# Kernel tuning notes

Hardware: AMD Instinct MI355X
Metric: run time of the kernel (lower is better)

## Reference

```python
import jax, jax.numpy as jnp
import numpy as np

B, S, D, E, K = 64, 1024, 1024, 8, 2
Z_COEF = 1e-3      # router_z_loss_coef
AUX_COEF = 1e-3    # router_aux_loss_coef


def setup_inputs() -> dict:
    key = jax.random.key(0)
    k1, k2, k3 = jax.random.split(key, 3)
    x = jax.random.normal(k1, (B, S, D), dtype=jnp.float32)
    # xavier-uniform-ish init for query weight, randn for expert keys (as in torch init)
    lim_q = float(np.sqrt(6.0 / (D + D)))
    Wq = jax.random.uniform(k2, (D, D), dtype=jnp.float32, minval=-lim_q, maxval=lim_q)
    bq = jnp.zeros((D,), dtype=jnp.float32)
    lim_k = float(np.sqrt(6.0 / (E + D)))
    key_emb = jax.random.uniform(k3, (E, D), dtype=jnp.float32, minval=-lim_k, maxval=lim_k)
    return {"x": x, "Wq": Wq, "bq": bq, "key_emb": key_emb}


def reference(x, Wq, bq, key_emb):
    b, s, d = x.shape
    e = key_emb.shape[0]
    scale = d ** (-0.5)

    # q = Linear(x); attn over expert keys
    q = jnp.einsum('bsd,od->bso', x, Wq) + bq              # [B,S,D]
    attn_scores = jnp.einsum('bsd,ed->bse', q, key_emb) * scale  # [B,S,E]
    attn_weights = jax.nn.softmax(attn_scores, axis=-1)    # [B,S,E]

    # per-batch expert scores, top-k selection, scatter mask
    scores = attn_weights.mean(axis=1)                     # [B,E]
    top_k_scores, top_k_indices = jax.lax.top_k(scores, K)  # [B,K]
    mask2d = jnp.zeros_like(scores).at[jnp.arange(b)[:, None], top_k_indices].set(1.0)  # [B,E]
    mask = jnp.broadcast_to(mask2d[:, None, :], (b, s, e))  # [B,S,E]

    # routing loss: KL(load-balance) + entropy-style aux
    total_tokens = b * s
    expert_usage_prob = mask2d.sum(axis=0) * (s / total_tokens)   # == mask.sum((0,1))/total
    ideal_prob = jnp.full((e,), 1.0 / e, dtype=scores.dtype)
    # F.kl_div(log_input, target, reduction='batchmean'): sum(t*(log t - log_in))/batch(=E)
    kl = jnp.sum(ideal_prob * (jnp.log(ideal_prob) - jnp.log(expert_usage_prob))) / e
    aux = jnp.mean(attn_weights * jnp.log(attn_weights + 1e-9))
    router_loss = Z_COEF * kl + AUX_COEF * aux

    return mask, top_k_indices, router_loss
```

## Files before the change

### kernel.cpp

```cpp
#include <hip/hip_runtime.h>
#include <math.h>

#define W2OFF  0
#define B2OFF  8192
#define SCOFF  8200
#define AUXOFF 8712
#define ZCNT   513

__global__ __launch_bounds__(256) void k0_prep(const float* __restrict__ bq,
                                               const float* __restrict__ key,
                                               float* __restrict__ ws) {
    __shared__ float part[256 * 8];
    int tid = threadIdx.x;
    #pragma unroll
    for (int k = 0; k < 3; ++k) {
        int i = tid + 256 * k;
        if (i < ZCNT) ws[SCOFF + i] = 0.0f;
    }
    float p[8];
    #pragma unroll
    for (int e = 0; e < 8; ++e) p[e] = 0.0f;
    #pragma unroll
    for (int k = 0; k < 4; ++k) {
        int d = tid + 256 * k;
        float bv = bq[d];
        #pragma unroll
        for (int e = 0; e < 8; ++e) p[e] += bv * key[e * 1024 + d];
    }
    #pragma unroll
    for (int e = 0; e < 8; ++e) part[tid * 8 + e] = p[e];
    __syncthreads();
    if (tid < 8) {
        float s = 0.0f;
        for (int k = 0; k < 256; ++k) s += part[k * 8 + tid];
        ws[B2OFF + tid] = s;
    }
}

__global__ __launch_bounds__(256) void k1_w2(const float* __restrict__ Wq,
                                             const float* __restrict__ key,
                                             float* __restrict__ ws) {
    __shared__ __attribute__((aligned(16))) float keyl[8 * 1024];
    __shared__ float part[256 * 8];
    int tid = threadIdx.x;
    int blk = blockIdx.x;

    float4* kl4 = (float4*)keyl;
    const float4* kg4 = (const float4*)key;
    #pragma unroll
    for (int k = 0; k < 8; ++k) kl4[tid + 256 * k] = kg4[tid + 256 * k];
    __syncthreads();

    int dl = tid & 15;
    int og = tid >> 4;
    int d  = blk * 16 + dl;
    float acc[8];
    #pragma unroll
    for (int e = 0; e < 8; ++e) acc[e] = 0.0f;
    for (int oo = 0; oo < 64; ++oo) {
        int o = og * 64 + oo;
        float wv = Wq[o * 1024 + d];
        #pragma unroll
        for (int e = 0; e < 8; ++e) acc[e] += keyl[e * 1024 + o] * wv;
    }
    #pragma unroll
    for (int e = 0; e < 8; ++e) part[tid * 8 + e] = acc[e];
    __syncthreads();
    if (tid < 128) {
        int dl2 = tid >> 3, e = tid & 7;
        float s = 0.0f;
        #pragma unroll
        for (int g = 0; g < 16; ++g) s += part[(g * 16 + dl2) * 8 + e];
        ws[W2OFF + e * 1024 + blk * 16 + dl2] = s;
    }
}

__global__ __launch_bounds__(256) void k2_main(const float* __restrict__ x,
                                               float* __restrict__ ws) {
    __shared__ __attribute__((aligned(16))) float w2l[8 * 1024];
    __shared__ __attribute__((aligned(16))) float part[4 * 64 * 8];
    __shared__ __attribute__((aligned(16))) float sraw[64 * 8];

    int tid  = threadIdx.x;
    int blk  = blockIdx.x;
    int lane = tid & 63;
    int w    = tid >> 6;
    int batch = blk >> 4;
    int tb    = blk * 64;

    float4* wl4 = (float4*)w2l;
    const float4* wg4 = (const float4*)(ws + W2OFF);
    #pragma unroll
    for (int k = 0; k < 8; ++k) wl4[tid + 256 * k] = wg4[tid + 256 * k];
    __syncthreads();

    const float4* x4 = (const float4*)x;
    float* pw = part + w * 512;

    for (int p = 0; p < 4; ++p) {
        int lt0 = w * 16 + p * 4;
        int t0  = tb + lt0;
        float acc[4][8];
        #pragma unroll
        for (int j = 0; j < 4; ++j)
            #pragma unroll
            for (int e = 0; e < 8; ++e) acc[j][e] = 0.0f;

        #pragma unroll
        for (int i = 0; i < 4; ++i) {
            float4 xr[4];
            #pragma unroll
            for (int j = 0; j < 4; ++j)
                xr[j] = x4[(size_t)(t0 + j) * 256 + i * 64 + lane];
            #pragma unroll
            for (int e = 0; e < 8; ++e) {
                float4 w4 = wl4[e * 256 + i * 64 + lane];
                #pragma unroll
                for (int j = 0; j < 4; ++j)
                    acc[j][e] += w4.x * xr[j].x + w4.y * xr[j].y +
                                 w4.z * xr[j].z + w4.w * xr[j].w;
            }
        }

        #pragma unroll
        for (int j = 0; j < 4; ++j) {
            float4* pw4 = (float4*)(pw + lane * 8);
            pw4[0] = make_float4(acc[j][0], acc[j][1], acc[j][2], acc[j][3]);
            pw4[1] = make_float4(acc[j][4], acc[j][5], acc[j][6], acc[j][7]);
            int e = lane >> 3, r = lane & 7;
            float s = 0.0f;
            #pragma unroll
            for (int m = 0; m < 8; ++m) s += pw[(r + m * 8) * 8 + e];
            s += __shfl_xor(s, 1);
            s += __shfl_xor(s, 2);
            s += __shfl_xor(s, 4);
            if (r == 0) sraw[(lt0 + j) * 8 + e] = s;
        }
    }
    __syncthreads();

    if (tid < 64) {
        float4 a = ((float4*)sraw)[tid * 2];
        float4 b = ((float4*)sraw)[tid * 2 + 1];
        float s[8] = {a.x, a.y, a.z, a.w, b.x, b.y, b.z, b.w};
        const float scale = 0.03125f;
        #pragma unroll
        for (int e = 0; e < 8; ++e) s[e] = (s[e] + ws[B2OFF + e]) * scale;
        float mx = s[0];
        #pragma unroll
        for (int e = 1; e < 8; ++e) mx = fmaxf(mx, s[e]);
        float wgt[8], sum = 0.0f;
        #pragma unroll
        for (int e = 0; e < 8; ++e) { wgt[e] = expf(s[e] - mx); sum += wgt[e]; }
        float inv = 1.0f / sum;
        float aux = 0.0f;
        #pragma unroll
        for (int e = 0; e < 8; ++e) {
            wgt[e] *= inv;
            aux += wgt[e] * logf(wgt[e] + 1e-9f);
        }
        float* pw0 = part;
        float4* q4 = (float4*)(pw0 + tid * 8);
        q4[0] = make_float4(wgt[0], wgt[1], wgt[2], wgt[3]);
        q4[1] = make_float4(wgt[4], wgt[5], wgt[6], wgt[7]);
        int e = tid >> 3, r = tid & 7;
        float s2 = 0.0f;
        #pragma unroll
        for (int m = 0; m < 8; ++m) s2 += pw0[(r + m * 8) * 8 + e];
        s2 += __shfl_xor(s2, 1);
        s2 += __shfl_xor(s2, 2);
        s2 += __shfl_xor(s2, 4);
        if (r == 0) atomicAdd(&ws[SCOFF + batch * 8 + e], s2);
        aux += __shfl_xor(aux, 1);
        aux += __shfl_xor(aux, 2);
        aux += __shfl_xor(aux, 4);
        aux += __shfl_xor(aux, 8);
        aux += __shfl_xor(aux, 16);
        aux += __shfl_xor(aux, 32);
        if (tid == 0) atomicAdd(&ws[AUXOFF], aux);
    }
}

__device__ __forceinline__ void top2_of8(const float* v, int& i1, int& i2) {
    i1 = 0; float b1 = v[0];
    #pragma unroll
    for (int e = 1; e < 8; ++e) if (v[e] > b1) { b1 = v[e]; i1 = e; }
    i2 = -1; float b2 = -3.4e38f;
    #pragma unroll
    for (int e = 0; e < 8; ++e) if (e != i1 && v[e] > b2) { b2 = v[e]; i2 = e; }
}

__global__ __launch_bounds__(256) void k3_out(const float* __restrict__ ws,
                                              float* __restrict__ out) {
    int tid = threadIdx.x;
    int blk = blockIdx.x;
    int batch = blk >> 2;

    float v[8];
    #pragma unroll
    for (int e = 0; e < 8; ++e) v[e] = ws[SCOFF + batch * 8 + e];
    int i1, i2;
    top2_of8(v, i1, i2);

    float m[8];
    #pragma unroll
    for (int e = 0; e < 8; ++e) m[e] = (e == i1 || e == i2) ? 1.0f : 0.0f;
    int token = blk * 256 + tid;
    float4* o4 = (float4*)out;
    o4[token * 2]     = make_float4(m[0], m[1], m[2], m[3]);
    o4[token * 2 + 1] = make_float4(m[4], m[5], m[6], m[7]);

    if (blk == 0) {
        __shared__ int cnt[8];
        if (tid < 8) cnt[tid] = 0;
        __syncthreads();
        if (tid < 64) {
            float vv[8];
            #pragma unroll
            for (int e = 0; e < 8; ++e) vv[e] = ws[SCOFF + tid * 8 + e];
            int j1, j2;
            top2_of8(vv, j1, j2);
            out[524288 + tid * 2]     = (float)j1;
            out[524288 + tid * 2 + 1] = (float)j2;
            atomicAdd(&cnt[j1], 1);
            atomicAdd(&cnt[j2], 1);
        }
        __syncthreads();
        if (tid == 0) {
            float kl = 0.0f;
            #pragma unroll
            for (int e = 0; e < 8; ++e) {
                float usage = (float)cnt[e] / 64.0f;
                kl += 0.125f * (logf(0.125f) - logf(usage));
            }
            kl *= 0.125f;
            float aux = ws[AUXOFF] / 524288.0f;
            out[524416] = 1e-3f * kl + 1e-3f * aux;
        }
    }
}

extern "C" void kernel_launch(void* const* d_in, const int* in_sizes, int n_in,
                              void* d_out, int out_size, void* d_ws, size_t ws_size,
                              hipStream_t stream) {
    const float* x   = (const float*)d_in[0];
    const float* Wq  = (const float*)d_in[1];
    const float* bq  = (const float*)d_in[2];
    const float* key = (const float*)d_in[3];
    float* out = (float*)d_out;
    float* ws  = (float*)d_ws;

    k0_prep<<<1,    256, 0, stream>>>(bq, key, ws);
    k1_w2  <<<64,   256, 0, stream>>>(Wq, key, ws);
    k2_main<<<1024, 256, 0, stream>>>(x, ws);
    k3_out <<<256,  256, 0, stream>>>(ws, out);
}
```

Baseline: 387.7 us.

## Fuse prep kernels and fold top-k/mask output into main kernel via last-block counters

Merges the bias-projection prep into the W2 precompute kernel and folds the softmax, top-2 selection, mask write and loss finalisation into the main x-streaming kernel. The last block per batch, found with an atomic ticket counter, writes that batch's mask, and the last batch finalises the loss. Softmax is now computed per token across lanes with shuffles rather than serially by one wave, and a launch-bounds occupancy hint is added. This removes two kernel launches and a separate pass over the mask, at the cost of atomics, fences and a tail of work in the final blocks.

```diff
diff --git a/kernel.cpp b/kernel.cpp
--- a/kernel.cpp
+++ b/kernel.cpp
@@ -5,46 +5,28 @@
 #define B2OFF  8192
 #define SCOFF  8200
 #define AUXOFF 8712
-#define ZCNT   513
-
-__global__ __launch_bounds__(256) void k0_prep(const float* __restrict__ bq,
-                                               const float* __restrict__ key,
-                                               float* __restrict__ ws) {
-    __shared__ float part[256 * 8];
-    int tid = threadIdx.x;
-    #pragma unroll
-    for (int k = 0; k < 3; ++k) {
-        int i = tid + 256 * k;
-        if (i < ZCNT) ws[SCOFF + i] = 0.0f;
-    }
-    float p[8];
-    #pragma unroll
-    for (int e = 0; e < 8; ++e) p[e] = 0.0f;
-    #pragma unroll
-    for (int k = 0; k < 4; ++k) {
-        int d = tid + 256 * k;
-        float bv = bq[d];
-        #pragma unroll
-        for (int e = 0; e < 8; ++e) p[e] += bv * key[e * 1024 + d];
-    }
-    #pragma unroll
-    for (int e = 0; e < 8; ++e) part[tid * 8 + e] = p[e];
-    __syncthreads();
-    if (tid < 8) {
-        float s = 0.0f;
-        for (int k = 0; k < 256; ++k) s += part[k * 8 + tid];
-        ws[B2OFF + tid] = s;
-    }
-}
-
-__global__ __launch_bounds__(256) void k1_w2(const float* __restrict__ Wq,
-                                             const float* __restrict__ key,
-                                             float* __restrict__ ws) {
+#define TKOFF  8713
+#define GTOFF  8777
+#define CNTOFF 8778
+#define ZTOT   586
+
+__global__ __launch_bounds__(256) void k01_prep(const float* __restrict__ Wq,
+                                                const float* __restrict__ key,
+                                                const float* __restrict__ bq,
+                                                float* __restrict__ ws) {
     __shared__ __attribute__((aligned(16))) float keyl[8 * 1024];
     __shared__ float part[256 * 8];
     int tid = threadIdx.x;
     int blk = blockIdx.x;
 
+    if (blk == 0) {
+        #pragma unroll
+        for (int k = 0; k < 3; ++k) {
+            int i = tid + 256 * k;
+            if (i < ZTOT) ws[SCOFF + i] = 0.0f;
+        }
+    }
+
     float4* kl4 = (float4*)keyl;
     const float4* kg4 = (const float4*)key;
     #pragma unroll
@@ -73,13 +55,44 @@
         for (int g = 0; g < 16; ++g) s += part[(g * 16 + dl2) * 8 + e];
         ws[W2OFF + e * 1024 + blk * 16 + dl2] = s;
     }
-}
-
-__global__ __launch_bounds__(256) void k2_main(const float* __restrict__ x,
-                                               float* __restrict__ ws) {
+
+    if (blk == 0) {
+        __syncthreads();
+        float p[8];
+        #pragma unroll
+        for (int e = 0; e < 8; ++e) p[e] = 0.0f;
+        #pragma unroll
+        for (int k = 0; k < 4; ++k) {
+            int d2 = tid + 256 * k;
+            float bv = bq[d2];
+            #pragma unroll
+            for (int e = 0; e < 8; ++e) p[e] += bv * keyl[e * 1024 + d2];
+        }
+        #pragma unroll
+        for (int e = 0; e < 8; ++e) part[tid * 8 + e] = p[e];
+        __syncthreads();
+        if (tid < 8) {
+            float s = 0.0f;
+            for (int k = 0; k < 256; ++k) s += part[k * 8 + tid];
+            ws[B2OFF + tid] = s;
+        }
+    }
+}
+
+__device__ __forceinline__ void top2_of8(const float* v, int& i1, int& i2) {
+    i1 = 0; float b1 = v[0];
+    #pragma unroll
+    for (int e = 1; e < 8; ++e) if (v[e] > b1) { b1 = v[e]; i1 = e; }
+    i2 = -1; float b2 = -3.4e38f;
+    #pragma unroll
+    for (int e = 0; e < 8; ++e) if (e != i1 && v[e] > b2) { b2 = v[e]; i2 = e; }
+}
+
+__global__ __launch_bounds__(256, 4) void k2_all(const float* __restrict__ x,
+                                                 float* __restrict__ ws,
+                                                 float* __restrict__ out) {
     __shared__ __attribute__((aligned(16))) float w2l[8 * 1024];
     __shared__ __attribute__((aligned(16))) float part[4 * 64 * 8];
-    __shared__ __attribute__((aligned(16))) float sraw[64 * 8];
 
     int tid  = threadIdx.x;
     int blk  = blockIdx.x;
@@ -87,15 +100,19 @@
     int w    = tid >> 6;
     int batch = blk >> 4;
     int tb    = blk * 64;
+    int e = lane >> 3, r = lane & 7;
 
     float4* wl4 = (float4*)w2l;
     const float4* wg4 = (const float4*)(ws + W2OFF);
     #pragma unroll
     for (int k = 0; k < 8; ++k) wl4[tid + 256 * k] = wg4[tid + 256 * k];
+    float b2v = ws[B2OFF + e];
     __syncthreads();
 
     const float4* x4 = (const float4*)x;
     float* pw = part + w * 512;
+    const float scale = 0.03125f;
+    float sc_acc = 0.0f, aux_acc = 0.0f;
 
     for (int p = 0; p < 4; ++p) {
         int lt0 = w * 16 + p * 4;
@@ -104,7 +121,7 @@
         #pragma unroll
         for (int j = 0; j < 4; ++j)
             #pragma unroll
-            for (int e = 0; e < 8; ++e) acc[j][e] = 0.0f;
+            for (int ee = 0; ee < 8; ++ee) acc[j][ee] = 0.0f;
 
         #pragma unroll
         for (int i = 0; i < 4; ++i) {
@@ -113,12 +130,12 @@
             for (int j = 0; j < 4; ++j)
                 xr[j] = x4[(size_t)(t0 + j) * 256 + i * 64 + lane];
             #pragma unroll
-            for (int e = 0; e < 8; ++e) {
-                float4 w4 = wl4[e * 256 + i * 64 + lane];
+            for (int ee = 0; ee < 8; ++ee) {
+                float4 w4 = wl4[ee * 256 + i * 64 + lane];
                 #pragma unroll
                 for (int j = 0; j < 4; ++j)
-                    acc[j][e] += w4.x * xr[j].x + w4.y * xr[j].y +
-                                 w4.z * xr[j].z + w4.w * xr[j].w;
+                    acc[j][ee] += w4.x * xr[j].x + w4.y * xr[j].y +
+                                  w4.z * xr[j].z + w4.w * xr[j].w;
             }
         }
 
@@ -127,114 +144,88 @@
             float4* pw4 = (float4*)(pw + lane * 8);
             pw4[0] = make_float4(acc[j][0], acc[j][1], acc[j][2], acc[j][3]);
             pw4[1] = make_float4(acc[j][4], acc[j][5], acc[j][6], acc[j][7]);
-            int e = lane >> 3, r = lane & 7;
             float s = 0.0f;
             #pragma unroll
             for (int m = 0; m < 8; ++m) s += pw[(r + m * 8) * 8 + e];
             s += __shfl_xor(s, 1);
             s += __shfl_xor(s, 2);
             s += __shfl_xor(s, 4);
-            if (r == 0) sraw[(lt0 + j) * 8 + e] = s;
-        }
-    }
-    __syncthreads();
-
-    if (tid < 64) {
-        float4 a = ((float4*)sraw)[tid * 2];
-        float4 b = ((float4*)sraw)[tid * 2 + 1];
-        float s[8] = {a.x, a.y, a.z, a.w, b.x, b.y, b.z, b.w};
-        const float scale = 0.03125f;
-        #pragma unroll
-        for (int e = 0; e < 8; ++e) s[e] = (s[e] + ws[B2OFF + e]) * scale;
-        float mx = s[0];
-        #pragma unroll
-        for (int e = 1; e < 8; ++e) mx = fmaxf(mx, s[e]);
-        float wgt[8], sum = 0.0f;
-        #pragma unroll
-        for (int e = 0; e < 8; ++e) { wgt[e] = expf(s[e] - mx); sum += wgt[e]; }
-        float inv = 1.0f / sum;
-        float aux = 0.0f;
-        #pragma unroll
-        for (int e = 0; e < 8; ++e) {
-            wgt[e] *= inv;
-            aux += wgt[e] * logf(wgt[e] + 1e-9f);
-        }
-        float* pw0 = part;
-        float4* q4 = (float4*)(pw0 + tid * 8);
-        q4[0] = make_float4(wgt[0], wgt[1], wgt[2], wgt[3]);
-        q4[1] = make_float4(wgt[4], wgt[5], wgt[6], wgt[7]);
-        int e = tid >> 3, r = tid & 7;
-        float s2 = 0.0f;
-        #pragma unroll
-        for (int m = 0; m < 8; ++m) s2 += pw0[(r + m * 8) * 8 + e];
-        s2 += __shfl_xor(s2, 1);
-        s2 += __shfl_xor(s2, 2);
-        s2 += __shfl_xor(s2, 4);
-        if (r == 0) atomicAdd(&ws[SCOFF + batch * 8 + e], s2);
-        aux += __shfl_xor(aux, 1);
-        aux += __shfl_xor(aux, 2);
-        aux += __shfl_xor(aux, 4);
-        aux += __shfl_xor(aux, 8);
-        aux += __shfl_xor(aux, 16);
-        aux += __shfl_xor(aux, 32);
-        if (tid == 0) atomicAdd(&ws[AUXOFF], aux);
-    }
-}
-
-__device__ __forceinline__ void top2_of8(const float* v, int& i1, int& i2) {
-    i1 = 0; float b1 = v[0];
-    #pragma unroll
-    for (int e = 1; e < 8; ++e) if (v[e] > b1) { b1 = v[e]; i1 = e; }
-    i2 = -1; float b2 = -3.4e38f;
-    #pragma unroll
-    for (int e = 0; e < 8; ++e) if (e != i1 && v[e] > b2) { b2 = v[e]; i2 = e; }
-}
-
-__global__ __launch_bounds__(256) void k3_out(const float* __restrict__ ws,
-                                              float* __restrict__ out) {
-    int tid = threadIdx.x;
-    int blk = blockIdx.x;
-    int batch = blk >> 2;
-
+            float sv = (s + b2v) * scale;
+            float mx = sv;
+            mx = fmaxf(mx, __shfl_xor(mx, 8));
+            mx = fmaxf(mx, __shfl_xor(mx, 16));
+            mx = fmaxf(mx, __shfl_xor(mx, 32));
+            float ex = expf(sv - mx);
+            float sm = ex;
+            sm += __shfl_xor(sm, 8);
+            sm += __shfl_xor(sm, 16);
+            sm += __shfl_xor(sm, 32);
+            float wgt = ex / sm;
+            sc_acc  += wgt;
+            aux_acc += wgt * logf(wgt + 1e-9f);
+        }
+    }
+
+    if (r == 0) atomicAdd(&ws[SCOFF + batch * 8 + e], sc_acc);
+    #pragma unroll
+    for (int mk = 1; mk <= 32; mk <<= 1) aux_acc += __shfl_xor(aux_acc, mk);
+    if (lane == 0) atomicAdd(&ws[AUXOFF], aux_acc * 0.125f);
+
+    __syncthreads();
+    int* pflag = (int*)part;
+    if (tid == 0) {
+        __threadfence();
+        int old = atomicAdd((int*)ws + TKOFF + batch, 1);
+        pflag[0] = (old == 15) ? 1 : 0;
+    }
+    __syncthreads();
+    if (pflag[0] == 0) return;
+
+    __threadfence();
     float v[8];
     #pragma unroll
-    for (int e = 0; e < 8; ++e) v[e] = ws[SCOFF + batch * 8 + e];
+    for (int ee = 0; ee < 8; ++ee)
+        v[ee] = __hip_atomic_load(&ws[SCOFF + batch * 8 + ee],
+                                  __ATOMIC_ACQUIRE, __HIP_MEMORY_SCOPE_AGENT);
     int i1, i2;
     top2_of8(v, i1, i2);
-
-    float m[8];
-    #pragma unroll
-    for (int e = 0; e < 8; ++e) m[e] = (e == i1 || e == i2) ? 1.0f : 0.0f;
-    int token = blk * 256 + tid;
+    float4 mA = make_float4(i1 == 0 || i2 == 0 ? 1.f : 0.f,
+                            i1 == 1 || i2 == 1 ? 1.f : 0.f,
+                            i1 == 2 || i2 == 2 ? 1.f : 0.f,
+                            i1 == 3 || i2 == 3 ? 1.f : 0.f);
+    float4 mB = make_float4(i1 == 4 || i2 == 4 ? 1.f : 0.f,
+                            i1 == 5 || i2 == 5 ? 1.f : 0.f,
+                            i1 == 6 || i2 == 6 ? 1.f : 0.f,
+                            i1 == 7 || i2 == 7 ? 1.f : 0.f);
     float4* o4 = (float4*)out;
-    o4[token * 2]     = make_float4(m[0], m[1], m[2], m[3]);
-    o4[token * 2 + 1] = make_float4(m[4], m[5], m[6], m[7]);
-
-    if (blk == 0) {
-        __shared__ int cnt[8];
-        if (tid < 8) cnt[tid] = 0;
-        __syncthreads();
-        if (tid < 64) {
-            float vv[8];
-            #pragma unroll
-            for (int e = 0; e < 8; ++e) vv[e] = ws[SCOFF + tid * 8 + e];
-            int j1, j2;
-            top2_of8(vv, j1, j2);
-            out[524288 + tid * 2]     = (float)j1;
-            out[524288 + tid * 2 + 1] = (float)j2;
-            atomicAdd(&cnt[j1], 1);
-            atomicAdd(&cnt[j2], 1);
-        }
-        __syncthreads();
-        if (tid == 0) {
+    int base = batch * 1024;
+    #pragma unroll
+    for (int t = 0; t < 4; ++t) {
+        int token = base + t * 256 + tid;
+        o4[token * 2]     = mA;
+        o4[token * 2 + 1] = mB;
+    }
+    if (tid == 0) {
+        out[524288 + batch * 2]     = (float)i1;
+        out[524288 + batch * 2 + 1] = (float)i2;
+        atomicAdd((int*)ws + CNTOFF + i1, 1);
+        atomicAdd((int*)ws + CNTOFF + i2, 1);
+        __threadfence();
+        int g = atomicAdd((int*)ws + GTOFF, 1);
+        if (g == 63) {
+            __threadfence();
             float kl = 0.0f;
             #pragma unroll
-            for (int e = 0; e < 8; ++e) {
-                float usage = (float)cnt[e] / 64.0f;
+            for (int ee = 0; ee < 8; ++ee) {
+                int c = __hip_atomic_load((int*)ws + CNTOFF + ee,
+                                          __ATOMIC_ACQUIRE, __HIP_MEMORY_SCOPE_AGENT);
+                float usage = (float)c / 64.0f;
                 kl += 0.125f * (logf(0.125f) - logf(usage));
             }
             kl *= 0.125f;
-            float aux = ws[AUXOFF] / 524288.0f;
+            float aux = __hip_atomic_load(&ws[AUXOFF],
+                                          __ATOMIC_ACQUIRE, __HIP_MEMORY_SCOPE_AGENT)
+                        / 524288.0f;
             out[524416] = 1e-3f * kl + 1e-3f * aux;
         }
     }
@@ -250,8 +241,6 @@
     float* out = (float*)d_out;
     float* ws  = (float*)d_ws;
 
-    k0_prep<<<1,    256, 0, stream>>>(bq, key, ws);
-    k1_w2  <<<64,   256, 0, stream>>>(Wq, key, ws);
-    k2_main<<<1024, 256, 0, stream>>>(x, ws);
-    k3_out <<<256,  256, 0, stream>>>(ws, out);
-}
+    k01_prep<<<64,   256, 0, stream>>>(Wq, key, bq, ws);
+    k2_all  <<<1024, 256, 0, stream>>>(x, ws, out);
+}
```

Result: slower. 829.3 us (+113.9%).

## Merge prep kernels and fuse per-token softmax into wave-level reduction epilogue

Applied to the files above, without the earlier changes.

The single-block bias-projection kernel is folded into the W2 kernel, with block 0 also zeroing the accumulators and computing the bias dot product from the key data already in shared memory, so one launch is removed. In the main kernel, the per-token softmax, aux-entropy and score accumulation now run inside every wave with shuffles, replacing the final 64-thread serial epilogue and its extra barrier. The shared-memory partial layout is XOR-swizzled to cut bank conflicts. The trade-off is more atomics per block (one per wave instead of one per block) and a serialized tail on block 0 of the prep kernel.

```diff
diff --git a/kernel.cpp b/kernel.cpp
--- a/kernel.cpp
+++ b/kernel.cpp
@@ -5,45 +5,24 @@
 #define B2OFF  8192
 #define SCOFF  8200
 #define AUXOFF 8712
-#define ZCNT   513
-
-__global__ __launch_bounds__(256) void k0_prep(const float* __restrict__ bq,
-                                               const float* __restrict__ key,
-                                               float* __restrict__ ws) {
-    __shared__ float part[256 * 8];
-    int tid = threadIdx.x;
-    #pragma unroll
-    for (int k = 0; k < 3; ++k) {
-        int i = tid + 256 * k;
-        if (i < ZCNT) ws[SCOFF + i] = 0.0f;
-    }
-    float p[8];
-    #pragma unroll
-    for (int e = 0; e < 8; ++e) p[e] = 0.0f;
-    #pragma unroll
-    for (int k = 0; k < 4; ++k) {
-        int d = tid + 256 * k;
-        float bv = bq[d];
-        #pragma unroll
-        for (int e = 0; e < 8; ++e) p[e] += bv * key[e * 1024 + d];
-    }
-    #pragma unroll
-    for (int e = 0; e < 8; ++e) part[tid * 8 + e] = p[e];
-    __syncthreads();
-    if (tid < 8) {
-        float s = 0.0f;
-        for (int k = 0; k < 256; ++k) s += part[k * 8 + tid];
-        ws[B2OFF + tid] = s;
-    }
-}
-
-__global__ __launch_bounds__(256) void k1_w2(const float* __restrict__ Wq,
-                                             const float* __restrict__ key,
-                                             float* __restrict__ ws) {
+#define ZTOT   513
+
+__global__ __launch_bounds__(256) void k01_prep(const float* __restrict__ Wq,
+                                                const float* __restrict__ key,
+                                                const float* __restrict__ bq,
+                                                float* __restrict__ ws) {
     __shared__ __attribute__((aligned(16))) float keyl[8 * 1024];
     __shared__ float part[256 * 8];
     int tid = threadIdx.x;
     int blk = blockIdx.x;
+
+    if (blk == 0) {
+        #pragma unroll
+        for (int k = 0; k < 3; ++k) {
+            int i = tid + 256 * k;
+            if (i < ZTOT) ws[SCOFF + i] = 0.0f;
+        }
+    }
 
     float4* kl4 = (float4*)keyl;
     const float4* kg4 = (const float4*)key;
@@ -73,13 +52,34 @@
         for (int g = 0; g < 16; ++g) s += part[(g * 16 + dl2) * 8 + e];
         ws[W2OFF + e * 1024 + blk * 16 + dl2] = s;
     }
+
+    if (blk == 0) {
+        __syncthreads();
+        float p[8];
+        #pragma unroll
+        for (int e = 0; e < 8; ++e) p[e] = 0.0f;
+        #pragma unroll
+        for (int k = 0; k < 4; ++k) {
+            int d2 = tid + 256 * k;
+            float bv = bq[d2];
+            #pragma unroll
+            for (int e = 0; e < 8; ++e) p[e] += bv * keyl[e * 1024 + d2];
+        }
+        #pragma unroll
+        for (int e = 0; e < 8; ++e) part[tid * 8 + e] = p[e];
+        __syncthreads();
+        if (tid < 8) {
+            float s = 0.0f;
+            for (int k = 0; k < 256; ++k) s += part[k * 8 + tid];
+            ws[B2OFF + tid] = s;
+        }
+    }
 }
 
 __global__ __launch_bounds__(256) void k2_main(const float* __restrict__ x,
                                                float* __restrict__ ws) {
     __shared__ __attribute__((aligned(16))) float w2l[8 * 1024];
     __shared__ __attribute__((aligned(16))) float part[4 * 64 * 8];
-    __shared__ __attribute__((aligned(16))) float sraw[64 * 8];
 
     int tid  = threadIdx.x;
     int blk  = blockIdx.x;
@@ -87,15 +87,20 @@
     int w    = tid >> 6;
     int batch = blk >> 4;
     int tb    = blk * 64;
+    int e = lane & 7;
+    int r = lane >> 3;
 
     float4* wl4 = (float4*)w2l;
     const float4* wg4 = (const float4*)(ws + W2OFF);
     #pragma unroll
     for (int k = 0; k < 8; ++k) wl4[tid + 256 * k] = wg4[tid + 256 * k];
+    float b2v = ws[B2OFF + e];
     __syncthreads();
 
     const float4* x4 = (const float4*)x;
     float* pw = part + w * 512;
+    const float scale = 0.03125f;
+    float sc_acc = 0.0f, aux_acc = 0.0f;
 
     for (int p = 0; p < 4; ++p) {
         int lt0 = w * 16 + p * 4;
@@ -104,7 +109,7 @@
         #pragma unroll
         for (int j = 0; j < 4; ++j)
             #pragma unroll
-            for (int e = 0; e < 8; ++e) acc[j][e] = 0.0f;
+            for (int c = 0; c < 8; ++c) acc[j][c] = 0.0f;
 
         #pragma unroll
         for (int i = 0; i < 4; ++i) {
@@ -113,72 +118,47 @@
             for (int j = 0; j < 4; ++j)
                 xr[j] = x4[(size_t)(t0 + j) * 256 + i * 64 + lane];
             #pragma unroll
-            for (int e = 0; e < 8; ++e) {
-                float4 w4 = wl4[e * 256 + i * 64 + lane];
+            for (int c = 0; c < 8; ++c) {
+                float4 w4 = wl4[c * 256 + i * 64 + lane];
                 #pragma unroll
                 for (int j = 0; j < 4; ++j)
-                    acc[j][e] += w4.x * xr[j].x + w4.y * xr[j].y +
+                    acc[j][c] += w4.x * xr[j].x + w4.y * xr[j].y +
                                  w4.z * xr[j].z + w4.w * xr[j].w;
             }
         }
 
         #pragma unroll
         for (int j = 0; j < 4; ++j) {
-            float4* pw4 = (float4*)(pw + lane * 8);
-            pw4[0] = make_float4(acc[j][0], acc[j][1], acc[j][2], acc[j][3]);
-            pw4[1] = make_float4(acc[j][4], acc[j][5], acc[j][6], acc[j][7]);
-            int e = lane >> 3, r = lane & 7;
+            #pragma unroll
+            for (int c = 0; c < 8; ++c)
+                pw[c * 64 + (lane ^ (c << 3))] = acc[j][c];
             float s = 0.0f;
             #pragma unroll
-            for (int m = 0; m < 8; ++m) s += pw[(r + m * 8) * 8 + e];
-            s += __shfl_xor(s, 1);
-            s += __shfl_xor(s, 2);
-            s += __shfl_xor(s, 4);
-            if (r == 0) sraw[(lt0 + j) * 8 + e] = s;
-        }
-    }
-    __syncthreads();
-
-    if (tid < 64) {
-        float4 a = ((float4*)sraw)[tid * 2];
-        float4 b = ((float4*)sraw)[tid * 2 + 1];
-        float s[8] = {a.x, a.y, a.z, a.w, b.x, b.y, b.z, b.w};
-        const float scale = 0.03125f;
-        #pragma unroll
-        for (int e = 0; e < 8; ++e) s[e] = (s[e] + ws[B2OFF + e]) * scale;
-        float mx = s[0];
-        #pragma unroll
-        for (int e = 1; e < 8; ++e) mx = fmaxf(mx, s[e]);
-        float wgt[8], sum = 0.0f;
-        #pragma unroll
-        for (int e = 0; e < 8; ++e) { wgt[e] = expf(s[e] - mx); sum += wgt[e]; }
-        float inv = 1.0f / sum;
-        float aux = 0.0f;
-        #pragma unroll
-        for (int e = 0; e < 8; ++e) {
-            wgt[e] *= inv;
-            aux += wgt[e] * logf(wgt[e] + 1e-9f);
-        }
-        float* pw0 = part;
-        float4* q4 = (float4*)(pw0 + tid * 8);
-        q4[0] = make_float4(wgt[0], wgt[1], wgt[2], wgt[3]);
-        q4[1] = make_float4(wgt[4], wgt[5], wgt[6], wgt[7]);
-        int e = tid >> 3, r = tid & 7;
-        float s2 = 0.0f;
-        #pragma unroll
-        for (int m = 0; m < 8; ++m) s2 += pw0[(r + m * 8) * 8 + e];
-        s2 += __shfl_xor(s2, 1);
-        s2 += __shfl_xor(s2, 2);
-        s2 += __shfl_xor(s2, 4);
-        if (r == 0) atomicAdd(&ws[SCOFF + batch * 8 + e], s2);
-        aux += __shfl_xor(aux, 1);
-        aux += __shfl_xor(aux, 2);
-        aux += __shfl_xor(aux, 4);
-        aux += __shfl_xor(aux, 8);
-        aux += __shfl_xor(aux, 16);
-        aux += __shfl_xor(aux, 32);
-        if (tid == 0) atomicAdd(&ws[AUXOFF], aux);
-    }
+            for (int m = 0; m < 8; ++m)
+                s += pw[e * 64 + ((r + 8 * m) ^ (e << 3))];
+            s += __shfl_xor(s, 8);
+            s += __shfl_xor(s, 16);
+            s += __shfl_xor(s, 32);
+            float sv = (s + b2v) * scale;
+            float mx = sv;
+            mx = fmaxf(mx, __shfl_xor(mx, 1));
+            mx = fmaxf(mx, __shfl_xor(mx, 2));
+            mx = fmaxf(mx, __shfl_xor(mx, 4));
+            float ex = expf(sv - mx);
+            float sm = ex;
+            sm += __shfl_xor(sm, 1);
+            sm += __shfl_xor(sm, 2);
+            sm += __shfl_xor(sm, 4);
+            float wgt = ex / sm;
+            sc_acc  += wgt;
+            aux_acc += wgt * logf(wgt + 1e-9f);
+        }
+    }
+
+    if (r == 0) atomicAdd(&ws[SCOFF + batch * 8 + e], sc_acc);
+    #pragma unroll
+    for (int mk = 1; mk <= 32; mk <<= 1) aux_acc += __shfl_xor(aux_acc, mk);
+    if (lane == 0) atomicAdd(&ws[AUXOFF], aux_acc * 0.125f);
 }
 
 __device__ __forceinline__ void top2_of8(const float* v, int& i1, int& i2) {
@@ -250,8 +230,7 @@
     float* out = (float*)d_out;
     float* ws  = (float*)d_ws;
 
-    k0_prep<<<1,    256, 0, stream>>>(bq, key, ws);
-    k1_w2  <<<64,   256, 0, stream>>>(Wq, key, ws);
+    k01_prep<<<64,   256, 0, stream>>>(Wq, key, bq, ws);
     k2_main<<<1024, 256, 0, stream>>>(x, ws);
     k3_out <<<256,  256, 0, stream>>>(ws, out);
 }
```

Measured after the change: 410.1 us. +5.8%, slower.
